# Kernel optimization log

Hardware: AMD Instinct MI355X
Metric: run time of the kernel (lower is better)

The kernel has to match this reference:

```python
import jax, jax.numpy as jnp
import numpy as np


def _pairwise_dist(p, t):
    # p: [B, N, 3], t: [B, M, 3] -> Euclidean distances [B, N, M]
    # ||p - t||^2 = ||p||^2 + ||t||^2 - 2 p.t  (avoids [B,N,M,3] intermediate)
    p2 = jnp.sum(p * p, axis=-1)  # [B, N]
    t2 = jnp.sum(t * t, axis=-1)  # [B, M]
    cross = jnp.einsum('bnd,bmd->bnm', p, t)  # [B, N, M]
    d2 = p2[:, :, None] + t2[:, None, :] - 2.0 * cross
    return jnp.sqrt(jnp.maximum(d2, 0.0))


def setup_inputs() -> dict:
    key = jax.random.key(0)
    k1, k2 = jax.random.split(key)
    pred = jax.random.normal(k1, (4, 3, 8192), dtype=jnp.float32)
    target = jax.random.normal(k2, (4, 3, 8192), dtype=jnp.float32)
    return {"pred": pred, "target": target}


def reference(pred, target):
    # pred, target: [B, 3, N] channel-first point clouds
    p = jnp.swapaxes(pred, 2, 1)    # [B, N, 3]
    t = jnp.swapaxes(target, 2, 1)  # [B, M, 3]
    dist = _pairwise_dist(p, t)     # [B, N, M]
    min_p_to_t = jnp.min(dist, axis=2).mean()
    min_t_to_p = jnp.min(dist, axis=1).mean()
    return min_p_to_t + min_t_to_p
```

## Files before the change

kernel.cpp:

```cpp
#include <hip/hip_runtime.h>


typedef __attribute__((ext_vector_type(8)))  short    bf16x8;
typedef __attribute__((ext_vector_type(16))) float    f32x16;
typedef __attribute__((ext_vector_type(4)))  unsigned uint32x4;

constexpr int NPTS   = 8192;
constexpr int COLS_W = 128;
constexpr int COLS_B = COLS_W * 4;
constexpr int N_CG   = NPTS / COLS_B;
constexpr int NSPLIT = 8;
constexpr int SROWS  = NPTS / NSPLIT;
constexpr int STEPS  = SROWS / 32;

__device__ inline float hi16f(float f) {
    return __uint_as_float(__float_as_uint(f) & 0xFFFF0000u);
}
__device__ inline unsigned pack2(float lo_src, float hi_src) {
    return __builtin_amdgcn_perm(__float_as_uint(hi_src),
                                 __float_as_uint(lo_src), 0x07060302u);
}

__global__ __launch_bounds__(256, 4) void chamfer_v6(
    const float* __restrict__ pred, const float* __restrict__ targ,
    float* __restrict__ part)
{
    const int lane = threadIdx.x & 63;
    const int wv   = threadIdx.x >> 6;
    const int l31  = lane & 31;
    const int g    = lane >> 5;
    const int mg   = blockIdx.x * 4 + wv;
    const int ns   = blockIdx.y;
    const int db   = blockIdx.z;
    const int dir  = db & 1, b = db >> 1;

    const float* F = (dir ? targ : pred) + (size_t)b * 3 * NPTS;
    const float* S = (dir ? pred : targ) + (size_t)b * 3 * NPTS;
    const unsigned ONE2 = 0x3F803F80u;

    auto build_bf = [&](int j) -> bf16x8 {
        int c = mg * COLS_W + j * 32 + l31;
        float x = F[c], y = F[NPTS + c], z = F[2 * NPTS + c];
        float f2  = fmaf(x, x, fmaf(y, y, z * z));
        float m2x = -2.f * x, m2y = -2.f * y, m2z = -2.f * z;
        uint32x4 d;
        if (g == 0) {
            float f2l  = f2  - hi16f(f2);
            float m2xl = m2x - hi16f(m2x);
            d[0] = ONE2;
            d[1] = pack2(f2, f2l);
            d[2] = pack2(m2x, m2xl);
            d[3] = pack2(m2x, m2y);
        } else {
            float m2yl = m2y - hi16f(m2y);
            float m2zl = m2z - hi16f(m2z);
            d[0] = pack2(m2yl, m2y);
            d[1] = pack2(m2z, m2zl);
            d[2] = pack2(m2z, 0.f);
            d[3] = 0u;
        }
        return __builtin_bit_cast(bf16x8, d);
    };
    bf16x8 bf0 = build_bf(0), bf1 = build_bf(1);
    bf16x8 bf2 = build_bf(2), bf3 = build_bf(3);

    auto build_af = [&](float x, float y, float z) -> bf16x8 {
        float s2 = fmaf(x, x, fmaf(y, y, z * z));
        uint32x4 d;
        if (g == 0) {
            float s2l = s2 - hi16f(s2);
            float xl  = x  - hi16f(x);
            d[0] = pack2(s2, s2l);
            d[1] = ONE2;
            d[2] = pack2(x, x);
            d[3] = pack2(xl, y);
        } else {
            float yl = y - hi16f(y);
            float zl = z - hi16f(z);
            d[0] = pack2(y, yl);
            d[1] = pack2(z, z);
            d[2] = pack2(zl, 0.f);
            d[3] = 0u;
        }
        return __builtin_bit_cast(bf16x8, d);
    };

    f32x16 zero;
    #pragma unroll
    for (int i = 0; i < 16; ++i) zero[i] = 0.f;

    const float INF = __int_as_float(0x7F800000);
    float a0 = INF, a1 = INF, a2 = INF, a3 = INF;

    auto tree = [](float acc, const f32x16& c) -> float {
        float t0 = fminf(fminf(c[0],  c[1]),  c[2]);
        float t1 = fminf(fminf(c[3],  c[4]),  c[5]);
        float t2 = fminf(fminf(c[6],  c[7]),  c[8]);
        float t3 = fminf(fminf(c[9],  c[10]), c[11]);
        float t4 = fminf(fminf(c[12], c[13]), c[14]);
        float r0 = fminf(fminf(t0, t1), t2);
        float r1 = fminf(fminf(t3, t4), c[15]);
        return fminf(fminf(r0, r1), acc);
    };

    const float* S0 = S + (size_t)ns * SROWS + l31;
    const float* S1 = S0 + NPTS;
    const float* S2 = S0 + 2 * NPTS;

    float cx = S0[0], cy = S1[0], cz = S2[0];
    for (int s = 0; s < STEPS; ++s) {
        float nx = 0.f, ny = 0.f, nz = 0.f;
        if (s + 1 < STEPS) {
            int o = (s + 1) * 32;
            nx = S0[o]; ny = S1[o]; nz = S2[o];
        }
        bf16x8 af = build_af(cx, cy, cz);
        f32x16 c0 = __builtin_amdgcn_mfma_f32_32x32x16_bf16(af, bf0, zero, 0, 0, 0);
        f32x16 c1 = __builtin_amdgcn_mfma_f32_32x32x16_bf16(af, bf1, zero, 0, 0, 0);
        a0 = tree(a0, c0);
        c0 = __builtin_amdgcn_mfma_f32_32x32x16_bf16(af, bf2, zero, 0, 0, 0);
        a1 = tree(a1, c1);
        c1 = __builtin_amdgcn_mfma_f32_32x32x16_bf16(af, bf3, zero, 0, 0, 0);
        a2 = tree(a2, c0);
        a3 = tree(a3, c1);
        cx = nx; cy = ny; cz = nz;
    }

    a0 = fminf(a0, __shfl_xor(a0, 32));
    a1 = fminf(a1, __shfl_xor(a1, 32));
    a2 = fminf(a2, __shfl_xor(a2, 32));
    a3 = fminf(a3, __shfl_xor(a3, 32));

    if (lane < 32) {
        float* dst = part + ((size_t)db * NSPLIT + ns) * NPTS + (size_t)mg * COLS_W;
        dst[l31]      = a0;
        dst[32 + l31] = a1;
        dst[64 + l31] = a2;
        dst[96 + l31] = a3;
    }
}

__global__ __launch_bounds__(256) void reduce_k(
    const float* __restrict__ part, float* __restrict__ out)
{
    int tid = blockIdx.x * 256 + threadIdx.x;
    int db  = tid >> 13;
    int m   = tid & (NPTS - 1);
    const float* base = part + (size_t)db * NSPLIT * NPTS + m;
    float v = base[0];
    #pragma unroll
    for (int nsh = 1; nsh < NSPLIT; ++nsh)
        v = fminf(v, base[(size_t)nsh * NPTS]);
    float d = sqrtf(fmaxf(v, 0.f)) * (1.0f / 32768.0f);
    for (int off = 32; off; off >>= 1) d += __shfl_down(d, off);
    __shared__ float wsum[4];
    if ((threadIdx.x & 63) == 0) wsum[threadIdx.x >> 6] = d;
    __syncthreads();
    if (threadIdx.x == 0) atomicAdd(out, wsum[0] + wsum[1] + wsum[2] + wsum[3]);
}

extern "C" void kernel_launch(void* const* d_in, const int* in_sizes, int n_in,
                              void* d_out, int out_size, void* d_ws, size_t ws_size,
                              hipStream_t stream) {
    const float* pred = (const float*)d_in[0];
    const float* targ = (const float*)d_in[1];
    float* out  = (float*)d_out;
    float* part = (float*)d_ws;

    hipMemsetAsync(d_out, 0, sizeof(float), stream);

    dim3 grid(N_CG, NSPLIT, 8);
    chamfer_v6<<<grid, 256, 0, stream>>>(pred, targ, part);

    reduce_k<<<(8 * NPTS) / 256, 256, 0, stream>>>(part, out);
}
```

Baseline: 80.85 us.

## Widen per-wave column tile to 256 and double row splits

```diff
diff --git a/kernel.cpp b/kernel.cpp
--- a/kernel.cpp
+++ b/kernel.cpp
@@ -6,10 +6,10 @@
 typedef __attribute__((ext_vector_type(4)))  unsigned uint32x4;
 
 constexpr int NPTS   = 8192;
-constexpr int COLS_W = 128;
+constexpr int COLS_W = 256;
 constexpr int COLS_B = COLS_W * 4;
 constexpr int N_CG   = NPTS / COLS_B;
-constexpr int NSPLIT = 8;
+constexpr int NSPLIT = 16;
 constexpr int SROWS  = NPTS / NSPLIT;
 constexpr int STEPS  = SROWS / 32;
 
@@ -21,14 +21,14 @@
                                  __float_as_uint(lo_src), 0x07060302u);
 }
 
-__global__ __launch_bounds__(256, 4) void chamfer_v6(
+__global__ __launch_bounds__(256, 4) void chamfer_v7(
     const float* __restrict__ pred, const float* __restrict__ targ,
     float* __restrict__ part)
 {
     const int lane = threadIdx.x & 63;
     const int wv   = threadIdx.x >> 6;
     const int l31  = lane & 31;
-    const int g    = lane >> 5;
+    const bool hi  = (lane >> 5) != 0;
     const int mg   = blockIdx.x * 4 + wv;
     const int ns   = blockIdx.y;
     const int db   = blockIdx.z;
@@ -38,50 +38,36 @@
     const float* S = (dir ? pred : targ) + (size_t)b * 3 * NPTS;
     const unsigned ONE2 = 0x3F803F80u;
 
-    auto build_bf = [&](int j) -> bf16x8 {
+    bf16x8 bfr[8];
+    #pragma unroll
+    for (int j = 0; j < 8; ++j) {
         int c = mg * COLS_W + j * 32 + l31;
         float x = F[c], y = F[NPTS + c], z = F[2 * NPTS + c];
         float f2  = fmaf(x, x, fmaf(y, y, z * z));
         float m2x = -2.f * x, m2y = -2.f * y, m2z = -2.f * z;
+        float f2l  = f2  - hi16f(f2);
+        float m2xl = m2x - hi16f(m2x);
+        float m2yl = m2y - hi16f(m2y);
+        float m2zl = m2z - hi16f(m2z);
         uint32x4 d;
-        if (g == 0) {
-            float f2l  = f2  - hi16f(f2);
-            float m2xl = m2x - hi16f(m2x);
-            d[0] = ONE2;
-            d[1] = pack2(f2, f2l);
-            d[2] = pack2(m2x, m2xl);
-            d[3] = pack2(m2x, m2y);
-        } else {
-            float m2yl = m2y - hi16f(m2y);
-            float m2zl = m2z - hi16f(m2z);
-            d[0] = pack2(m2yl, m2y);
-            d[1] = pack2(m2z, m2zl);
-            d[2] = pack2(m2z, 0.f);
-            d[3] = 0u;
-        }
-        return __builtin_bit_cast(bf16x8, d);
-    };
-    bf16x8 bf0 = build_bf(0), bf1 = build_bf(1);
-    bf16x8 bf2 = build_bf(2), bf3 = build_bf(3);
+        d[0] = hi ? pack2(m2yl, m2y) : ONE2;
+        d[1] = hi ? pack2(m2z, m2zl) : pack2(f2, f2l);
+        d[2] = hi ? pack2(m2z, 0.f)  : pack2(m2x, m2xl);
+        d[3] = hi ? 0u               : pack2(m2x, m2y);
+        bfr[j] = __builtin_bit_cast(bf16x8, d);
+    }
 
     auto build_af = [&](float x, float y, float z) -> bf16x8 {
-        float s2 = fmaf(x, x, fmaf(y, y, z * z));
+        float s2  = fmaf(x, x, fmaf(y, y, z * z));
+        float s2l = s2 - hi16f(s2);
+        float xl  = x - hi16f(x);
+        float yl  = y - hi16f(y);
+        float zl  = z - hi16f(z);
         uint32x4 d;
-        if (g == 0) {
-            float s2l = s2 - hi16f(s2);
-            float xl  = x  - hi16f(x);
-            d[0] = pack2(s2, s2l);
-            d[1] = ONE2;
-            d[2] = pack2(x, x);
-            d[3] = pack2(xl, y);
-        } else {
-            float yl = y - hi16f(y);
-            float zl = z - hi16f(z);
-            d[0] = pack2(y, yl);
-            d[1] = pack2(z, z);
-            d[2] = pack2(zl, 0.f);
-            d[3] = 0u;
-        }
+        d[0] = hi ? pack2(y, yl)  : pack2(s2, s2l);
+        d[1] = hi ? pack2(z, z)   : ONE2;
+        d[2] = hi ? pack2(zl, 0.f): pack2(x, x);
+        d[3] = hi ? 0u            : pack2(xl, y);
         return __builtin_bit_cast(bf16x8, d);
     };
 
@@ -91,6 +77,7 @@
 
     const float INF = __int_as_float(0x7F800000);
     float a0 = INF, a1 = INF, a2 = INF, a3 = INF;
+    float a4 = INF, a5 = INF, a6 = INF, a7 = INF;
 
     auto tree = [](float acc, const f32x16& c) -> float {
         float t0 = fminf(fminf(c[0],  c[1]),  c[2]);
@@ -107,36 +94,54 @@
     const float* S1 = S0 + NPTS;
     const float* S2 = S0 + 2 * NPTS;
 
+    auto step = [&](float x, float y, float z) {
+        bf16x8 af = build_af(x, y, z);
+        f32x16 c0 = __builtin_amdgcn_mfma_f32_32x32x16_bf16(af, bfr[0], zero, 0, 0, 0);
+        f32x16 c1 = __builtin_amdgcn_mfma_f32_32x32x16_bf16(af, bfr[1], zero, 0, 0, 0);
+        a0 = tree(a0, c0);
+        c0 = __builtin_amdgcn_mfma_f32_32x32x16_bf16(af, bfr[2], zero, 0, 0, 0);
+        a1 = tree(a1, c1);
+        c1 = __builtin_amdgcn_mfma_f32_32x32x16_bf16(af, bfr[3], zero, 0, 0, 0);
+        a2 = tree(a2, c0);
+        c0 = __builtin_amdgcn_mfma_f32_32x32x16_bf16(af, bfr[4], zero, 0, 0, 0);
+        a3 = tree(a3, c1);
+        c1 = __builtin_amdgcn_mfma_f32_32x32x16_bf16(af, bfr[5], zero, 0, 0, 0);
+        a4 = tree(a4, c0);
+        c0 = __builtin_amdgcn_mfma_f32_32x32x16_bf16(af, bfr[6], zero, 0, 0, 0);
+        a5 = tree(a5, c1);
+        c1 = __builtin_amdgcn_mfma_f32_32x32x16_bf16(af, bfr[7], zero, 0, 0, 0);
+        a6 = tree(a6, c0);
+        a7 = tree(a7, c1);
+    };
+
     float cx = S0[0], cy = S1[0], cz = S2[0];
-    for (int s = 0; s < STEPS; ++s) {
-        float nx = 0.f, ny = 0.f, nz = 0.f;
-        if (s + 1 < STEPS) {
-            int o = (s + 1) * 32;
-            nx = S0[o]; ny = S1[o]; nz = S2[o];
-        }
-        bf16x8 af = build_af(cx, cy, cz);
-        f32x16 c0 = __builtin_amdgcn_mfma_f32_32x32x16_bf16(af, bf0, zero, 0, 0, 0);
-        f32x16 c1 = __builtin_amdgcn_mfma_f32_32x32x16_bf16(af, bf1, zero, 0, 0, 0);
-        a0 = tree(a0, c0);
-        c0 = __builtin_amdgcn_mfma_f32_32x32x16_bf16(af, bf2, zero, 0, 0, 0);
-        a1 = tree(a1, c1);
-        c1 = __builtin_amdgcn_mfma_f32_32x32x16_bf16(af, bf3, zero, 0, 0, 0);
-        a2 = tree(a2, c0);
-        a3 = tree(a3, c1);
+    for (int s = 0; s < STEPS - 1; ++s) {
+        int o = (s + 1) * 32;
+        float nx = S0[o], ny = S1[o], nz = S2[o];
+        step(cx, cy, cz);
         cx = nx; cy = ny; cz = nz;
     }
+    step(cx, cy, cz);
 
     a0 = fminf(a0, __shfl_xor(a0, 32));
     a1 = fminf(a1, __shfl_xor(a1, 32));
     a2 = fminf(a2, __shfl_xor(a2, 32));
     a3 = fminf(a3, __shfl_xor(a3, 32));
+    a4 = fminf(a4, __shfl_xor(a4, 32));
+    a5 = fminf(a5, __shfl_xor(a5, 32));
+    a6 = fminf(a6, __shfl_xor(a6, 32));
+    a7 = fminf(a7, __shfl_xor(a7, 32));
 
     if (lane < 32) {
         float* dst = part + ((size_t)db * NSPLIT + ns) * NPTS + (size_t)mg * COLS_W;
-        dst[l31]      = a0;
-        dst[32 + l31] = a1;
-        dst[64 + l31] = a2;
-        dst[96 + l31] = a3;
+        dst[l31]       = a0;
+        dst[32  + l31] = a1;
+        dst[64  + l31] = a2;
+        dst[96  + l31] = a3;
+        dst[128 + l31] = a4;
+        dst[160 + l31] = a5;
+        dst[192 + l31] = a6;
+        dst[224 + l31] = a7;
     }
 }
 
@@ -170,7 +175,7 @@
     hipMemsetAsync(d_out, 0, sizeof(float), stream);
 
     dim3 grid(N_CG, NSPLIT, 8);
-    chamfer_v6<<<grid, 256, 0, stream>>>(pred, targ, part);
+    chamfer_v7<<<grid, 256, 0, stream>>>(pred, targ, part);
 
     reduce_k<<<(8 * NPTS) / 256, 256, 0, stream>>>(part, out);
 }
```

Result: no change. 81.17 us (+0.4%).
